# Kernel tuning notes

Measured on AMD Instinct MI355X. Metric: run time of the kernel, lower is better.

The kernel has to match this reference:

```python
import jax, jax.numpy as jnp
import numpy as np

B = 8192
E, IN, H, OUT = 6, 2086, 512, 512


def setup_inputs() -> dict:
    key = jax.random.key(0)
    ks = jax.random.split(key, 6)
    wb1 = np.sqrt(6.0 / (IN * H))
    wb2 = np.sqrt(6.0 / (H * H))
    wb3 = np.sqrt(6.0 / (H * OUT))
    return {
        "frame_prev": jax.random.normal(ks[0], (B, 1830), dtype=jnp.float32),
        "I": jax.random.normal(ks[1], (B, 256), dtype=jnp.float32),
        "blending_coef": jax.nn.softmax(jax.random.normal(ks[2], (B, E), dtype=jnp.float32), axis=-1),
        "w1": jax.random.uniform(ks[3], (E, IN, H), jnp.float32, -wb1, wb1),
        "b1": jnp.zeros((E, H), jnp.float32),
        "w2": jax.random.uniform(ks[4], (E, H, H), jnp.float32, -wb2, wb2),
        "b2": jnp.zeros((E, H), jnp.float32),
        "w3": jax.random.uniform(ks[5], (E, H, OUT), jnp.float32, -wb3, wb3),
        "b3": jnp.zeros((E, OUT), jnp.float32),
    }


def _blended_linear(h, coef, w, b):
    # Algebraically identical to sum_e coef[b,e] * (h @ w[e]) + coef @ b,
    # which equals (h @ sum_e coef[b,e] w[e]) + coef @ b as in the torch code,
    # but avoids materializing the [B, in, out] blended weight tensor.
    per_expert = jnp.einsum('bi,eio->beo', h, w)   # [B, E, out]
    return jnp.einsum('be,beo->bo', coef, per_expert) + coef @ b


def reference(frame_prev, I, blending_coef, w1, b1, w2, b2, w3, b3):
    h0 = jnp.concatenate([frame_prev, I], axis=1)          # [B, 2086]
    h1 = jax.nn.elu(_blended_linear(h0, blending_coef, w1, b1))
    h2 = jax.nn.elu(_blended_linear(h1, blending_coef, w2, b2))
    h3 = jax.nn.elu(_blended_linear(h2, blending_coef, w3, b3))
    return h3
```

## Files before the change

### kernel.cpp

```cpp
#include <hip/hip_runtime.h>
#include <hip/hip_bf16.h>
#include <cstdint>
#include <cstddef>

typedef __attribute__((ext_vector_type(4))) float f32x4;
typedef __attribute__((ext_vector_type(8))) short bf16x8;

#define E_  6
#define B_  8192
#define H_  512

__device__ __forceinline__ unsigned short f32_to_bf16_rn(float f) {
    uint32_t u = __float_as_uint(f);
    uint32_t r = (u + 0x7fffu + ((u >> 16) & 1u)) >> 16;
    return (unsigned short)r;
}
__device__ __forceinline__ float bf16_to_f32(unsigned short h) {
    return __uint_as_float(((uint32_t)h) << 16);
}

__global__ void convert_h_kernel(const float* __restrict__ srcA, const float* __restrict__ srcB,
                                 int splitA, int K_in, int NK, int nchunks,
                                 short* __restrict__ dhi, short* __restrict__ dlo)
{
    int c = blockIdx.x * 256 + threadIdx.x;
    if (c >= nchunks) return;
    int lane  = c & 63;
    int mf    = (c >> 6) & 7;
    int rest  = c >> 9;
    int kstep = rest % NK;
    int bm    = rest / NK;
    int b  = bm * 128 + mf * 16 + (lane & 15);
    int k0 = kstep * 32 + (lane >> 4) * 8;

    union { short s[8]; int4 v; } uh, ul;
#pragma unroll
    for (int j = 0; j < 8; ++j) {
        int k = k0 + j;
        float v = 0.f;
        if (k < K_in) {
            v = (k < splitA) ? srcA[(size_t)b * splitA + k]
                             : srcB[(size_t)b * (K_in - splitA) + (k - splitA)];
        }
        unsigned short h = f32_to_bf16_rn(v);
        float rem = v - bf16_to_f32(h);
        unsigned short l = f32_to_bf16_rn(rem);
        uh.s[j] = (short)h;
        ul.s[j] = (short)l;
    }
    *reinterpret_cast<int4*>(dhi + (size_t)c * 8) = uh.v;
    *reinterpret_cast<int4*>(dlo + (size_t)c * 8) = ul.v;
}

__global__ void convert_w_kernel(const float* __restrict__ w, int K_in, int NK, int nchunks,
                                 short* __restrict__ dhi, short* __restrict__ dlo)
{
    int c = blockIdx.x * 256 + threadIdx.x;
    if (c >= nchunks) return;
    int lane  = c & 63;
    int nf    = (c >> 6) & 3;
    int rest  = c >> 8;
    int kstep = rest % NK;
    int eb    = rest / NK;
    int bn    = eb & 7;
    int e     = eb >> 3;
    int o  = bn * 64 + nf * 16 + (lane & 15);
    int k0 = kstep * 32 + (lane >> 4) * 8;

    union { short s[8]; int4 v; } uh, ul;
#pragma unroll
    for (int j = 0; j < 8; ++j) {
        int k = k0 + j;
        float v = 0.f;
        if (k < K_in) v = w[((size_t)e * K_in + k) * H_ + o];
        unsigned short h = f32_to_bf16_rn(v);
        float rem = v - bf16_to_f32(h);
        unsigned short l = f32_to_bf16_rn(rem);
        uh.s[j] = (short)h;
        ul.s[j] = (short)l;
    }
    *reinterpret_cast<int4*>(dhi + (size_t)c * 8) = uh.v;
    *reinterpret_cast<int4*>(dlo + (size_t)c * 8) = ul.v;
}

__global__ __launch_bounds__(256, 2)
void blend_gemm_kernel(const short* __restrict__ Ah, const short* __restrict__ Al,
                       const short* __restrict__ Bh, const short* __restrict__ Bl,
                       const float* __restrict__ coef, const float* __restrict__ bias,
                       float* __restrict__ out, int NK)
{
    __shared__ __align__(16) short lds[28672];

    const int tid  = threadIdx.x;
    const int lane = tid & 63;
    const int wave = tid >> 6;
    const int wm   = wave >> 1;
    const int wn   = wave & 1;
    const int blk  = blockIdx.x;
    const int bn   = blk & 7;
    const int bm   = blk >> 3;

    const size_t abase     = (size_t)bm * NK * 4096;
    const size_t bstride_e = (size_t)8 * NK * 2048;
    const size_t bbase0    = (size_t)bn * NK * 2048;

    auto issueA = [&](int s) {
        const size_t a_s = abase + (size_t)s * 4096;
        short* dst = &lds[(s & 1) * 8192];
#pragma unroll
        for (int i = 0; i < 4; ++i) {
            const int ch = wave * 4 + i;
            const short* g = (ch < 8) ? (Ah + a_s + ch * 512)
                                      : (Al + a_s + (ch - 8) * 512);
            __builtin_amdgcn_global_load_lds(
                (const __attribute__((address_space(1))) short*)(g + lane * 8),
                (__attribute__((address_space(3))) short*)(dst + ch * 512),
                16, 0, 0);
        }
    };
    auto issueB = [&](int ebuf, int eexp, int s) {
        const size_t off = (size_t)eexp * bstride_e + bbase0 + (size_t)s * 2048;
        short* dst = &lds[16384 + ebuf * 4096];
#pragma unroll
        for (int i = 0; i < 2; ++i) {
            const int ch = wave * 2 + i;
            const short* g = (ch < 4) ? (Bh + off + ch * 512)
                                      : (Bl + off + (ch - 4) * 512);
            __builtin_amdgcn_global_load_lds(
                (const __attribute__((address_space(1))) short*)(g + lane * 8),
                (__attribute__((address_space(3))) short*)(dst + ch * 512),
                16, 0, 0);
        }
    };

    const f32x4 zero = {0.f, 0.f, 0.f, 0.f};
    f32x4 acc[E_][4][2];
#pragma unroll
    for (int e = 0; e < E_; ++e)
#pragma unroll
        for (int mf = 0; mf < 4; ++mf)
#pragma unroll
            for (int nf = 0; nf < 2; ++nf) acc[e][mf][nf] = zero;

    bf16x8 ah[4], al4[4];

    __builtin_amdgcn_sched_barrier(0);
    issueA(0);
    issueB(0, 0, 0);
    issueB(1, 1, 0);
    __builtin_amdgcn_sched_barrier(0);

    for (int s = 0; s < NK; ++s) {
        const bool lastS = (s == NK - 1);
#pragma unroll
        for (int e = 0; e < 6; ++e) {
            if (e < 4) {
                asm volatile("s_waitcnt vmcnt(2) lgkmcnt(0)" ::: "memory");
            } else if (e == 4) {
                if (!lastS) asm volatile("s_waitcnt vmcnt(6) lgkmcnt(0)" ::: "memory");
                else        asm volatile("s_waitcnt vmcnt(2) lgkmcnt(0)" ::: "memory");
            } else {
                if (!lastS) asm volatile("s_waitcnt vmcnt(6) lgkmcnt(0)" ::: "memory");
                else        asm volatile("s_waitcnt vmcnt(0) lgkmcnt(0)" ::: "memory");
            }
            __builtin_amdgcn_s_barrier();
            __builtin_amdgcn_sched_barrier(0);

            if (e < 4) {
                issueB((e + 2) % 3, e + 2, s);
            } else if (!lastS) {
                issueB((e + 2) % 3, e - 4, s + 1);
            }
            if (e == 3 && !lastS) issueA(s + 1);
            __builtin_amdgcn_sched_barrier(0);

            if (e == 0) {
                const short* Ab = &lds[(s & 1) * 8192];
#pragma unroll
                for (int mf = 0; mf < 4; ++mf) {
                    ah[mf]  = *reinterpret_cast<const bf16x8*>(&Ab[((wm * 4 + mf) * 64 + lane) * 8]);
                    al4[mf] = *reinterpret_cast<const bf16x8*>(&Ab[((8 + wm * 4 + mf) * 64 + lane) * 8]);
                }
            }
            const short* Bb = &lds[16384 + (e % 3) * 4096];
            bf16x8 bh[2], bl[2];
#pragma unroll
            for (int nf = 0; nf < 2; ++nf) {
                bh[nf] = *reinterpret_cast<const bf16x8*>(&Bb[((wn * 2 + nf) * 64 + lane) * 8]);
                bl[nf] = *reinterpret_cast<const bf16x8*>(&Bb[((4 + wn * 2 + nf) * 64 + lane) * 8]);
            }

            __builtin_amdgcn_s_setprio(1);
#pragma unroll
            for (int mf = 0; mf < 4; ++mf)
#pragma unroll
                for (int nf = 0; nf < 2; ++nf) {
                    acc[e][mf][nf] = __builtin_amdgcn_mfma_f32_16x16x32_bf16(ah[mf],  bh[nf], acc[e][mf][nf], 0, 0, 0);
                    acc[e][mf][nf] = __builtin_amdgcn_mfma_f32_16x16x32_bf16(ah[mf],  bl[nf], acc[e][mf][nf], 0, 0, 0);
                    acc[e][mf][nf] = __builtin_amdgcn_mfma_f32_16x16x32_bf16(al4[mf], bh[nf], acc[e][mf][nf], 0, 0, 0);
                }
            __builtin_amdgcn_s_setprio(0);
            __builtin_amdgcn_sched_barrier(0);
        }
    }

    float bb[E_][2];
#pragma unroll
    for (int nf = 0; nf < 2; ++nf) {
        const int col = bn * 64 + wn * 32 + nf * 16 + (lane & 15);
#pragma unroll
        for (int e = 0; e < E_; ++e) bb[e][nf] = bias[e * H_ + col];
    }

#pragma unroll
    for (int mf = 0; mf < 4; ++mf) {
        const int r0 = bm * 128 + wm * 64 + mf * 16 + (lane >> 4) * 4;
#pragma unroll
        for (int q = 0; q < 4; ++q) {
            const int r = r0 + q;
            const float2* c2 = reinterpret_cast<const float2*>(coef + (size_t)r * E_);
            float2 ca = c2[0], cb = c2[1], cc = c2[2];
            float cf[E_] = {ca.x, ca.y, cb.x, cb.y, cc.x, cc.y};
#pragma unroll
            for (int nf = 0; nf < 2; ++nf) {
                const int col = bn * 64 + wn * 32 + nf * 16 + (lane & 15);
                float v = 0.f;
#pragma unroll
                for (int e = 0; e < E_; ++e)
                    v += cf[e] * (acc[e][mf][nf][q] + bb[e][nf]);
                v = v > 0.f ? v : expm1f(v);
                out[(size_t)r * H_ + col] = v;
            }
        }
    }
}

extern "C" void kernel_launch(void* const* d_in, const int* in_sizes, int n_in,
                              void* d_out, int out_size, void* d_ws, size_t ws_size,
                              hipStream_t stream)
{
    if (n_in < 9) return;
    const float* frame = (const float*)d_in[0];
    const float* Iin   = (const float*)d_in[1];
    const float* coef  = (const float*)d_in[2];
    const float* w1    = (const float*)d_in[3];
    const float* b1    = (const float*)d_in[4];
    const float* w2    = (const float*)d_in[5];
    const float* b2    = (const float*)d_in[6];
    const float* w3    = (const float*)d_in[7];
    const float* b3    = (const float*)d_in[8];
    float* out = (float*)d_out;
    char* ws = (char*)d_ws;

    const int NK1 = 66;
    const int NK2 = 16;

    const size_t A0sz = (size_t)8192 * 2112 * 2;
    const size_t W1sz = (size_t)6 * 2112 * 512 * 2;
    const size_t W2sz = (size_t)6 * 512 * 512 * 2;
    const size_t H1f  = (size_t)8192 * 512 * 4;
    const size_t H1b  = (size_t)8192 * 512 * 2;

    const size_t need = 2 * A0sz + 2 * W1sz + 4 * W2sz + H1f + 2 * H1b;
    if (ws_size < need) return;

    short* A0h = (short*)(ws);
    short* A0l = (short*)(ws + A0sz);
    short* w1h = (short*)(ws + 2 * A0sz);
    short* w1l = (short*)(ws + 2 * A0sz + W1sz);
    short* w2h = (short*)(ws + 2 * A0sz + 2 * W1sz);
    short* w2l = (short*)(ws + 2 * A0sz + 2 * W1sz + W2sz);
    short* w3h = (short*)(ws + 2 * A0sz + 2 * W1sz + 2 * W2sz);
    short* w3l = (short*)(ws + 2 * A0sz + 2 * W1sz + 3 * W2sz);
    float* h1  = (float*)(ws + 2 * A0sz + 2 * W1sz + 4 * W2sz);
    short* h1h = (short*)((char*)h1 + H1f);
    short* h1l = (short*)((char*)h1 + H1f + H1b);
    float* h2  = (float*)(ws);
    short* h2h = (short*)(ws + H1f);
    short* h2l = (short*)(ws + H1f + H1b);

    {
        int nch = (8192 / 128) * NK1 * 8 * 64;
        convert_h_kernel<<<nch / 256, 256, 0, stream>>>(frame, Iin, 1830, 2086, NK1, nch, A0h, A0l);
    }
    {
        int nch = 6 * 8 * NK1 * 4 * 64;
        convert_w_kernel<<<nch / 256, 256, 0, stream>>>(w1, 2086, NK1, nch, w1h, w1l);
    }
    {
        int nch = 6 * 8 * NK2 * 4 * 64;
        convert_w_kernel<<<nch / 256, 256, 0, stream>>>(w2, 512, NK2, nch, w2h, w2l);
        convert_w_kernel<<<nch / 256, 256, 0, stream>>>(w3, 512, NK2, nch, w3h, w3l);
    }

    const int grid = 512;
    blend_gemm_kernel<<<grid, 256, 0, stream>>>(A0h, A0l, w1h, w1l, coef, b1, h1, NK1);
    {
        int nch = (8192 / 128) * NK2 * 8 * 64;
        convert_h_kernel<<<nch / 256, 256, 0, stream>>>(h1, nullptr, 512, 512, NK2, nch, h1h, h1l);
    }
    blend_gemm_kernel<<<grid, 256, 0, stream>>>(h1h, h1l, w2h, w2l, coef, b2, h2, NK2);
    {
        int nch = (8192 / 128) * NK2 * 8 * 64;
        convert_h_kernel<<<nch / 256, 256, 0, stream>>>(h2, nullptr, 512, 512, NK2, nch, h2h, h2l);
    }
    blend_gemm_kernel<<<grid, 256, 0, stream>>>(h2h, h2l, w3h, w3l, coef, b3, out, NK2);
}
```

Measured before the change: 569.6 us.

## Process experts in pairs per barrier phase and vectorize input conversion loads

The GEMM main loop now handles two experts per pipeline phase (three phases per k-step instead of six). Each phase loads a larger B tile for both experts into one of three LDS slots, and the A tile is single-buffered and reloaded in phase 1. This halves the number of barriers and waitcnt stalls per k-step and gives each phase more MFMA work to hide load latency, at the cost of more LDS use (64KB) and a tighter reuse window for the A buffer. Separately, the activation-conversion kernel reads its fp32 inputs as float2 vectors when a chunk does not straddle the concat boundary.

```diff
diff --git a/kernel.cpp b/kernel.cpp
--- a/kernel.cpp
+++ b/kernel.cpp
@@ -33,17 +33,39 @@
     int b  = bm * 128 + mf * 16 + (lane & 15);
     int k0 = kstep * 32 + (lane >> 4) * 8;
 
+    float vv[8];
+    if (k0 + 7 < splitA) {
+        const float* p = srcA + (size_t)b * splitA + k0;
+#pragma unroll
+        for (int h = 0; h < 4; ++h) {
+            float2 x = *reinterpret_cast<const float2*>(p + 2 * h);
+            vv[2 * h] = x.x; vv[2 * h + 1] = x.y;
+        }
+    } else if (k0 >= splitA && k0 + 7 < K_in) {
+        const float* p = srcB + (size_t)b * (K_in - splitA) + (k0 - splitA);
+#pragma unroll
+        for (int h = 0; h < 4; ++h) {
+            float2 x = *reinterpret_cast<const float2*>(p + 2 * h);
+            vv[2 * h] = x.x; vv[2 * h + 1] = x.y;
+        }
+    } else {
+#pragma unroll
+        for (int j = 0; j < 8; ++j) {
+            int k = k0 + j;
+            float v = 0.f;
+            if (k < K_in) {
+                v = (k < splitA) ? srcA[(size_t)b * splitA + k]
+                                 : srcB[(size_t)b * (K_in - splitA) + (k - splitA)];
+            }
+            vv[j] = v;
+        }
+    }
+
     union { short s[8]; int4 v; } uh, ul;
 #pragma unroll
     for (int j = 0; j < 8; ++j) {
-        int k = k0 + j;
-        float v = 0.f;
-        if (k < K_in) {
-            v = (k < splitA) ? srcA[(size_t)b * splitA + k]
-                             : srcB[(size_t)b * (K_in - splitA) + (k - splitA)];
-        }
-        unsigned short h = f32_to_bf16_rn(v);
-        float rem = v - bf16_to_f32(h);
+        unsigned short h = f32_to_bf16_rn(vv[j]);
+        float rem = vv[j] - bf16_to_f32(h);
         unsigned short l = f32_to_bf16_rn(rem);
         uh.s[j] = (short)h;
         ul.s[j] = (short)l;
@@ -89,7 +111,7 @@
                        const float* __restrict__ coef, const float* __restrict__ bias,
                        float* __restrict__ out, int NK)
 {
-    __shared__ __align__(16) short lds[28672];
+    __shared__ __align__(16) short lds[32768];
 
     const int tid  = threadIdx.x;
     const int lane = tid & 63;
@@ -106,7 +128,7 @@
 
     auto issueA = [&](int s) {
         const size_t a_s = abase + (size_t)s * 4096;
-        short* dst = &lds[(s & 1) * 8192];
+        short* dst = &lds[0];
 #pragma unroll
         for (int i = 0; i < 4; ++i) {
             const int ch = wave * 4 + i;
@@ -118,14 +140,16 @@
                 16, 0, 0);
         }
     };
-    auto issueB = [&](int ebuf, int eexp, int s) {
-        const size_t off = (size_t)eexp * bstride_e + bbase0 + (size_t)s * 2048;
-        short* dst = &lds[16384 + ebuf * 4096];
-#pragma unroll
-        for (int i = 0; i < 2; ++i) {
-            const int ch = wave * 2 + i;
-            const short* g = (ch < 4) ? (Bh + off + ch * 512)
-                                      : (Bl + off + (ch - 4) * 512);
+    auto issueB = [&](int slot, int p, int s) {
+        short* dst = &lds[8192 + slot * 8192];
+        const size_t base = bbase0 + (size_t)s * 2048;
+#pragma unroll
+        for (int i = 0; i < 4; ++i) {
+            const int ch   = wave * 4 + i;
+            const int eSub = ch >> 3;
+            const int t    = ch & 7;
+            const size_t off = (size_t)(2 * p + eSub) * bstride_e + base + (size_t)(t & 3) * 512;
+            const short* g = ((t < 4) ? Bh : Bl) + off;
             __builtin_amdgcn_global_load_lds(
                 (const __attribute__((address_space(1))) short*)(g + lane * 8),
                 (__attribute__((address_space(3))) short*)(dst + ch * 512),
@@ -145,60 +169,66 @@
     bf16x8 ah[4], al4[4];
 
     __builtin_amdgcn_sched_barrier(0);
+    issueB(0, 0, 0);
     issueA(0);
-    issueB(0, 0, 0);
     issueB(1, 1, 0);
     __builtin_amdgcn_sched_barrier(0);
 
     for (int s = 0; s < NK; ++s) {
         const bool lastS = (s == NK - 1);
 #pragma unroll
-        for (int e = 0; e < 6; ++e) {
-            if (e < 4) {
-                asm volatile("s_waitcnt vmcnt(2) lgkmcnt(0)" ::: "memory");
-            } else if (e == 4) {
-                if (!lastS) asm volatile("s_waitcnt vmcnt(6) lgkmcnt(0)" ::: "memory");
-                else        asm volatile("s_waitcnt vmcnt(2) lgkmcnt(0)" ::: "memory");
+        for (int p = 0; p < 3; ++p) {
+            if (p == 0) {
+                asm volatile("s_waitcnt vmcnt(4) lgkmcnt(0)" ::: "memory");
+            } else if (p == 1) {
+                asm volatile("s_waitcnt vmcnt(4) lgkmcnt(0)" ::: "memory");
             } else {
-                if (!lastS) asm volatile("s_waitcnt vmcnt(6) lgkmcnt(0)" ::: "memory");
+                if (!lastS) asm volatile("s_waitcnt vmcnt(8) lgkmcnt(0)" ::: "memory");
                 else        asm volatile("s_waitcnt vmcnt(0) lgkmcnt(0)" ::: "memory");
             }
             __builtin_amdgcn_s_barrier();
             __builtin_amdgcn_sched_barrier(0);
 
-            if (e < 4) {
-                issueB((e + 2) % 3, e + 2, s);
-            } else if (!lastS) {
-                issueB((e + 2) % 3, e - 4, s + 1);
-            }
-            if (e == 3 && !lastS) issueA(s + 1);
+            if (p == 0) {
+                issueB(2, 2, s);
+            } else if (p == 1) {
+                if (!lastS) { issueB(0, 0, s + 1); issueA(s + 1); }
+            } else {
+                if (!lastS) issueB(1, 1, s + 1);
+            }
             __builtin_amdgcn_sched_barrier(0);
 
-            if (e == 0) {
-                const short* Ab = &lds[(s & 1) * 8192];
+            if (p == 0) {
+                const short* Ab = &lds[0];
 #pragma unroll
                 for (int mf = 0; mf < 4; ++mf) {
                     ah[mf]  = *reinterpret_cast<const bf16x8*>(&Ab[((wm * 4 + mf) * 64 + lane) * 8]);
                     al4[mf] = *reinterpret_cast<const bf16x8*>(&Ab[((8 + wm * 4 + mf) * 64 + lane) * 8]);
                 }
             }
-            const short* Bb = &lds[16384 + (e % 3) * 4096];
-            bf16x8 bh[2], bl[2];
-#pragma unroll
-            for (int nf = 0; nf < 2; ++nf) {
-                bh[nf] = *reinterpret_cast<const bf16x8*>(&Bb[((wn * 2 + nf) * 64 + lane) * 8]);
-                bl[nf] = *reinterpret_cast<const bf16x8*>(&Bb[((4 + wn * 2 + nf) * 64 + lane) * 8]);
-            }
+            const short* Bb = &lds[8192 + p * 8192];
+            bf16x8 bh[2][2], bl[2][2];
+#pragma unroll
+            for (int eSub = 0; eSub < 2; ++eSub)
+#pragma unroll
+                for (int nf = 0; nf < 2; ++nf) {
+                    bh[eSub][nf] = *reinterpret_cast<const bf16x8*>(&Bb[((eSub * 8 +     wn * 2 + nf) * 64 + lane) * 8]);
+                    bl[eSub][nf] = *reinterpret_cast<const bf16x8*>(&Bb[((eSub * 8 + 4 + wn * 2 + nf) * 64 + lane) * 8]);
+                }
 
             __builtin_amdgcn_s_setprio(1);
 #pragma unroll
-            for (int mf = 0; mf < 4; ++mf)
-#pragma unroll
-                for (int nf = 0; nf < 2; ++nf) {
-                    acc[e][mf][nf] = __builtin_amdgcn_mfma_f32_16x16x32_bf16(ah[mf],  bh[nf], acc[e][mf][nf], 0, 0, 0);
-                    acc[e][mf][nf] = __builtin_amdgcn_mfma_f32_16x16x32_bf16(ah[mf],  bl[nf], acc[e][mf][nf], 0, 0, 0);
-                    acc[e][mf][nf] = __builtin_amdgcn_mfma_f32_16x16x32_bf16(al4[mf], bh[nf], acc[e][mf][nf], 0, 0, 0);
-                }
+            for (int eSub = 0; eSub < 2; ++eSub) {
+                const int e = 2 * p + eSub;
+#pragma unroll
+                for (int mf = 0; mf < 4; ++mf)
+#pragma unroll
+                    for (int nf = 0; nf < 2; ++nf) {
+                        acc[e][mf][nf] = __builtin_amdgcn_mfma_f32_16x16x32_bf16(ah[mf],  bh[eSub][nf], acc[e][mf][nf], 0, 0, 0);
+                        acc[e][mf][nf] = __builtin_amdgcn_mfma_f32_16x16x32_bf16(ah[mf],  bl[eSub][nf], acc[e][mf][nf], 0, 0, 0);
+                        acc[e][mf][nf] = __builtin_amdgcn_mfma_f32_16x16x32_bf16(al4[mf], bh[eSub][nf], acc[e][mf][nf], 0, 0, 0);
+                    }
+            }
             __builtin_amdgcn_s_setprio(0);
             __builtin_amdgcn_sched_barrier(0);
         }
```

Result: slower. 1.359 ms (+138.6%).
